# Performance work log

Hardware: AMD Instinct MI355X
Metric: run time of the kernel (lower is better)

Reference implementation:

```python
import jax, jax.numpy as jnp
import numpy as np

DIM = 768
NH = 12
HID = int(DIM * 1.5)  # 1152
B_, T_, W_ = 8, 8, 14
HW = 14 * 14
N = HW + 1
BT = B_ * T_


def _ln(x, g, b, eps=1e-5):
    m = jnp.mean(x, axis=-1, keepdims=True)
    v = jnp.var(x, axis=-1, keepdims=True)
    return (x - m) / jnp.sqrt(v + eps) * g + b


def _attn(x, wqkv, wproj, bproj, nh):
    # manual q@k^T -> softmax -> @v, as in the torch module (no qkv bias)
    b, n, c = x.shape
    hd = c // nh
    scale = hd ** -0.5
    qkv = (x @ wqkv.T).reshape(b, n, 3, nh, hd).transpose(2, 0, 3, 1, 4)
    q, k, v = qkv[0], qkv[1], qkv[2]
    a = jax.nn.softmax(jnp.einsum('bhnd,bhmd->bhnm', q, k) * scale, axis=-1)
    o = jnp.einsum('bhnm,bhmd->bhnd', a, v).transpose(0, 2, 1, 3).reshape(b, n, c)
    return o @ wproj.T + bproj


def setup_inputs() -> dict:
    key = jax.random.key(0)
    ks = jax.random.split(key, 16)
    s = 0.02
    d = {
        'x': jax.random.normal(ks[0], (BT, N, DIM), jnp.float32),
        'ln1_g': jnp.ones((DIM,), jnp.float32),
        'ln1_b': jnp.zeros((DIM,), jnp.float32),
        'qkv_w': jax.random.normal(ks[1], (3 * DIM, DIM), jnp.float32) * s,
        'proj_w': jax.random.normal(ks[2], (DIM, DIM), jnp.float32) * s,
        'proj_b': jnp.zeros((DIM,), jnp.float32),
        'tln_g': jnp.ones((DIM,), jnp.float32),
        'tln_b': jnp.zeros((DIM,), jnp.float32),
        'tqkv_w': jax.random.normal(ks[3], (3 * DIM, DIM), jnp.float32) * s,
        'tproj_w': jax.random.normal(ks[4], (DIM, DIM), jnp.float32) * s,
        'tproj_b': jnp.zeros((DIM,), jnp.float32),
        # module zero-inits temporal_fc; use small random so the branch is exercised
        'tfc_w': jax.random.normal(ks[5], (DIM, DIM), jnp.float32) * s,
        'tfc_b': jnp.zeros((DIM,), jnp.float32),
        'ln2_g': jnp.ones((DIM,), jnp.float32),
        'ln2_b': jnp.zeros((DIM,), jnp.float32),
        'fc1_w': jax.random.normal(ks[6], (HID, DIM), jnp.float32) * s,
        'fc1_b': jnp.zeros((HID,), jnp.float32),
        'fc2_w': jax.random.normal(ks[7], (DIM, HID), jnp.float32) * s,
        'fc2_b': jnp.zeros((DIM,), jnp.float32),
        'B': B_, 'T': T_, 'W': W_,
    }
    return d


def reference(x, ln1_g, ln1_b, qkv_w, proj_w, proj_b,
              tln_g, tln_b, tqkv_w, tproj_w, tproj_b, tfc_w, tfc_b,
              ln2_g, ln2_b, fc1_w, fc1_b, fc2_w, fc2_b, B, T, W):
    bt, n, c = x.shape
    hw = n - 1  # spatial tokens (cls excluded)
    # temporal branch: (b t) hw m -> (b hw) t m
    xt = x[:, 1:, :].reshape(B, T, hw, c).transpose(0, 2, 1, 3).reshape(B * hw, T, c)
    xt = _attn(_ln(xt, tln_g, tln_b), tqkv_w, tproj_w, tproj_b, NH)
    xt = xt.reshape(B, hw, T, c).transpose(0, 2, 1, 3).reshape(bt, hw, c)
    xt = xt @ tfc_w.T + tfc_b
    x = x.at[:, 1:, :].add(xt)  # in-place += in torch
    # spatial attention + residual
    x = x + _attn(_ln(x, ln1_g, ln1_b), qkv_w, proj_w, proj_b, NH)
    # MLP + residual (exact GELU, matching nn.GELU default)
    h = jax.nn.gelu(_ln(x, ln2_g, ln2_b) @ fc1_w.T + fc1_b, approximate=False)
    x = x + (h @ fc2_w.T + fc2_b)
    return x
```

## Files before the change

kernel.cpp:

```cpp
#include <hip/hip_runtime.h>
#include <hip/hip_bf16.h>


#define DIM   768
#define NH    12
#define HD    64
#define HID   1152
#define B_    8
#define T_    8
#define HW_   196
#define NTOK  197
#define BT_   64
#define MROWS (BT_ * NTOK)
#define TROWS (B_ * HW_ * T_)

typedef __bf16 bf16x8 __attribute__((ext_vector_type(8)));
typedef float  f32x4  __attribute__((ext_vector_type(4)));

__device__ inline float bf2f(ushort u) { return __uint_as_float(((unsigned)u) << 16); }
__device__ inline ushort f2bf(float f) {
    unsigned u = __float_as_uint(f);
    unsigned r = (u + 0x7fffu + ((u >> 16) & 1u)) >> 16;
    return (ushort)r;
}

__device__ inline float wred_sum(float v) {
    #pragma unroll
    for (int m = 32; m; m >>= 1) v += __shfl_xor(v, m);
    return v;
}

__device__ __forceinline__ void gload_lds16(const void* g, void* l) {
    __builtin_amdgcn_global_load_lds(
        (const __attribute__((address_space(1))) unsigned int*)g,
        (__attribute__((address_space(3))) unsigned int*)l, 16, 0, 0);
}

__device__ __forceinline__ int xcd_lin(int gid, int nwg) {
    int q = nwg >> 3, r = nwg & 7;
    int xcd = gid & 7, idx = gid >> 3;
    return (xcd < r ? xcd * (q + 1) : r * (q + 1) + (xcd - r) * q) + idx;
}

#define MFMA16(a, b, c) __builtin_amdgcn_mfma_f32_16x16x32_bf16(a, b, c, 0, 0, 0)

__global__ __launch_bounds__(256) void cast_all(
    const float* s0, ushort* d0, int c0, const float* s1, ushort* d1, int c1,
    const float* s2, ushort* d2, int c2, const float* s3, ushort* d3, int c3,
    const float* s4, ushort* d4, int c4, const float* s5, ushort* d5, int c5,
    const float* s6, ushort* d6, int c6)
{
    int i = blockIdx.x * 256 + threadIdx.x;
    const float* s; ushort* d; int base;
    if      (i < c0) { s = s0; d = d0; base = 0;  }
    else if (i < c1) { s = s1; d = d1; base = c0; }
    else if (i < c2) { s = s2; d = d2; base = c1; }
    else if (i < c3) { s = s3; d = d3; base = c2; }
    else if (i < c4) { s = s4; d = d4; base = c3; }
    else if (i < c5) { s = s5; d = d5; base = c4; }
    else if (i < c6) { s = s6; d = d6; base = c5; }
    else return;
    int k = i - base;
    float4 a = *(const float4*)(s + (size_t)k * 8);
    float4 b = *(const float4*)(s + (size_t)k * 8 + 4);
    ushort o[8] = {f2bf(a.x), f2bf(a.y), f2bf(a.z), f2bf(a.w),
                   f2bf(b.x), f2bf(b.y), f2bf(b.z), f2bf(b.w)};
    *(uint4*)(d + (size_t)k * 8) = *(const uint4*)o;
}

__global__ __launch_bounds__(256) void init_cls(const float* __restrict__ x, float* __restrict__ out)
{
    int i = blockIdx.x * 256 + threadIdx.x;
    int r = i / 192, c = (i % 192) * 4;
    size_t off = ((size_t)r * NTOK) * DIM + c;
    *(float4*)(out + off) = *(const float4*)(x + off);
}

template <int KK>
__global__ __launch_bounds__(512, 1) void gemm256(
    const ushort* __restrict__ Ag, const ushort* __restrict__ Wg,
    ushort* __restrict__ Cg, int M, int N, int nm, int nn, int grp)
{
    __shared__ ushort As[2][256 * 64];
    __shared__ ushort Bs[2][256 * 64];

    const int tid  = threadIdx.x;
    const int lane = tid & 63, wid = tid >> 6;
    const int wr = wid >> 2, wc = wid & 3;
    const int fr = lane & 15, fq = lane >> 4;

    int lin = xcd_lin(blockIdx.x, nm * nn);
    int per = grp * nn;
    int g2 = lin / per, rem = lin % per;
    int bm = g2 * grp;
    int gm = nm - bm; if (gm > grp) gm = grp;
    const int m0 = (bm + rem % gm) * 256;
    const int n0 = (rem / gm) * 256;

    const int srow = wid * 8 + (lane >> 3);
    const int scol = 8 * ((lane & 7) ^ (lane >> 3));
    const ushort* aP[4]; const ushort* bP[4];
    #pragma unroll
    for (int j = 0; j < 4; ++j) {
        int ra = m0 + j * 64 + srow; if (ra >= M) ra = M - 1;
        aP[j] = Ag + (size_t)ra * KK + scol;
        bP[j] = Wg + (size_t)(n0 + j * 64 + srow) * KK + scol;
    }
    const int ldso = (wid * 8) * 64;

    f32x4 acc[8][4] = {};
    bf16x8 af[4][2], b0[2][2], b1[2][2];

    const int sw0 = (fq * 8) ^ ((fr & 7) * 8);
    const int sw1 = (32 + fq * 8) ^ ((fr & 7) * 8);

    #pragma unroll
    for (int j = 0; j < 4; ++j) gload_lds16(aP[j], &As[0][j * 4096 + ldso]);
    #pragma unroll
    for (int j = 0; j < 4; ++j) gload_lds16(bP[j], &Bs[0][j * 4096 + ldso]);

    constexpr int NT = KK / 64;
    #pragma unroll
    for (int t = 0; t < NT; ++t) {
        const int rb = t & 1, wb = rb ^ 1;
        const bool st = (t + 1 < NT);
        const int kw = (t + 1) * 64;

        asm volatile("s_waitcnt vmcnt(0)" ::: "memory");
        __builtin_amdgcn_s_barrier();
        __builtin_amdgcn_sched_barrier(0);

        #pragma unroll
        for (int mf = 0; mf < 4; ++mf) {
            af[mf][0] = *(const bf16x8*)&As[rb][(wr * 128 + mf * 16 + fr) * 64 + sw0];
            af[mf][1] = *(const bf16x8*)&As[rb][(wr * 128 + mf * 16 + fr) * 64 + sw1];
        }
        #pragma unroll
        for (int nf = 0; nf < 2; ++nf) {
            b0[nf][0] = *(const bf16x8*)&Bs[rb][(wc * 64 + nf * 16 + fr) * 64 + sw0];
            b0[nf][1] = *(const bf16x8*)&Bs[rb][(wc * 64 + nf * 16 + fr) * 64 + sw1];
        }
        if (st) {
            #pragma unroll
            for (int j = 0; j < 4; ++j) gload_lds16(aP[j] + kw, &As[wb][j * 4096 + ldso]);
        }
        asm volatile("s_waitcnt lgkmcnt(0)" ::: "memory");
        __builtin_amdgcn_sched_barrier(0);
        __builtin_amdgcn_s_setprio(1);
        #pragma unroll
        for (int mf = 0; mf < 4; ++mf)
            #pragma unroll
            for (int nf = 0; nf < 2; ++nf) {
                acc[mf][nf] = MFMA16(af[mf][0], b0[nf][0], acc[mf][nf]);
                acc[mf][nf] = MFMA16(af[mf][1], b0[nf][1], acc[mf][nf]);
            }
        __builtin_amdgcn_s_setprio(0);
        __builtin_amdgcn_sched_barrier(0);

        #pragma unroll
        for (int nf = 0; nf < 2; ++nf) {
            b1[nf][0] = *(const bf16x8*)&Bs[rb][(wc * 64 + (nf + 2) * 16 + fr) * 64 + sw0];
            b1[nf][1] = *(const bf16x8*)&Bs[rb][(wc * 64 + (nf + 2) * 16 + fr) * 64 + sw1];
        }
        if (st) {
            #pragma unroll
            for (int j = 0; j < 4; ++j) gload_lds16(bP[j] + kw, &Bs[wb][j * 4096 + ldso]);
        }
        asm volatile("s_waitcnt lgkmcnt(0)" ::: "memory");
        __builtin_amdgcn_sched_barrier(0);
        __builtin_amdgcn_s_setprio(1);
        #pragma unroll
        for (int mf = 0; mf < 4; ++mf)
            #pragma unroll
            for (int nf = 0; nf < 2; ++nf) {
                acc[mf][nf + 2] = MFMA16(af[mf][0], b1[nf][0], acc[mf][nf + 2]);
                acc[mf][nf + 2] = MFMA16(af[mf][1], b1[nf][1], acc[mf][nf + 2]);
            }
        __builtin_amdgcn_s_setprio(0);
        __builtin_amdgcn_sched_barrier(0);

        #pragma unroll
        for (int mf = 0; mf < 4; ++mf) {
            af[mf][0] = *(const bf16x8*)&As[rb][(wr * 128 + 64 + mf * 16 + fr) * 64 + sw0];
            af[mf][1] = *(const bf16x8*)&As[rb][(wr * 128 + 64 + mf * 16 + fr) * 64 + sw1];
        }
        asm volatile("s_waitcnt lgkmcnt(0)" ::: "memory");
        __builtin_amdgcn_sched_barrier(0);
        __builtin_amdgcn_s_setprio(1);
        #pragma unroll
        for (int mf = 0; mf < 4; ++mf)
            #pragma unroll
            for (int nf = 0; nf < 2; ++nf) {
                acc[mf + 4][nf] = MFMA16(af[mf][0], b0[nf][0], acc[mf + 4][nf]);
                acc[mf + 4][nf] = MFMA16(af[mf][1], b0[nf][1], acc[mf + 4][nf]);
            }
        __builtin_amdgcn_s_setprio(0);
        __builtin_amdgcn_sched_barrier(0);

        __builtin_amdgcn_s_setprio(1);
        #pragma unroll
        for (int mf = 0; mf < 4; ++mf)
            #pragma unroll
            for (int nf = 0; nf < 2; ++nf) {
                acc[mf + 4][nf + 2] = MFMA16(af[mf][0], b1[nf][0], acc[mf + 4][nf + 2]);
                acc[mf + 4][nf + 2] = MFMA16(af[mf][1], b1[nf][1], acc[mf + 4][nf + 2]);
            }
        __builtin_amdgcn_s_setprio(0);
        __builtin_amdgcn_sched_barrier(0);
    }

    #pragma unroll
    for (int mf = 0; mf < 8; ++mf)
        #pragma unroll
        for (int e = 0; e < 4; ++e) {
            int row = m0 + wr * 128 + mf * 16 + fq * 4 + e;
            if (row >= M) continue;
            #pragma unroll
            for (int nf = 0; nf < 4; ++nf)
                Cg[(size_t)row * N + n0 + wc * 64 + nf * 16 + fr] = f2bf(acc[mf][nf][e]);
        }
}

enum { EPI_STORE = 0, EPI_BIAS_STORE = 1, EPI_BIAS_GELU = 2, EPI_BIAS_ADD = 3, EPI_BIAS_INIT_TFC = 4 };

template <int EPI, int KK>
__global__ __launch_bounds__(256) void gemm_bt(
    const ushort* __restrict__ Ag, const ushort* __restrict__ Wg,
    const float* __restrict__ bias, ushort* __restrict__ Cg,
    const float* __restrict__ xsrc, float* __restrict__ xf,
    int M, int N, int nm, int nn, int grp)
{
    __shared__ ushort As[2][128 * 64];
    __shared__ ushort Bs[2][128 * 64];

    const int tid  = threadIdx.x;
    const int lane = tid & 63, wid = tid >> 6;

    int lin = xcd_lin(blockIdx.x, nm * nn);
    int per = grp * nn;
    int g2 = lin / per, rem = lin % per;
    int bm = g2 * grp;
    int gm = nm - bm; if (gm > grp) gm = grp;
    const int m0 = (bm + rem % gm) * 128;
    const int n0 = (rem / gm) * 128;

    const int wm = (wid >> 1) * 64, wn = (wid & 1) * 64;
    const int fr = lane & 15, fq = lane >> 4;

    const int srow   = wid * 8 + (lane >> 3);
    const int scolsw = 8 * ((lane & 7) ^ (lane >> 3));
    const ushort* aSrc[4]; const ushort* bSrc[4];
    #pragma unroll
    for (int j = 0; j < 4; ++j) {
        int ra = m0 + j * 32 + srow; if (ra >= M) ra = M - 1;
        aSrc[j] = Ag + (size_t)ra * KK + scolsw;
        bSrc[j] = Wg + (size_t)(n0 + j * 32 + srow) * KK + scolsw;
    }

    f32x4 acc[4][4] = {};

    auto STAGE = [&](int buf, int k0) {
        #pragma unroll
        for (int j = 0; j < 4; ++j) {
            gload_lds16(aSrc[j] + k0, &As[buf][(j * 32 + wid * 8) * 64]);
            gload_lds16(bSrc[j] + k0, &Bs[buf][(j * 32 + wid * 8) * 64]);
        }
    };

    auto COMPUTE = [&](int buf) {
        #pragma unroll
        for (int ks = 0; ks < 2; ++ks) {
            bf16x8 af[4], bfr[4];
            #pragma unroll
            for (int i = 0; i < 4; ++i)
                af[i] = *(const bf16x8*)&As[buf][(wm + i * 16 + fr) * 64 +
                                                ((ks * 32 + fq * 8) ^ ((fr & 7) * 8))];
            #pragma unroll
            for (int j = 0; j < 4; ++j)
                bfr[j] = *(const bf16x8*)&Bs[buf][(wn + j * 16 + fr) * 64 +
                                                 ((ks * 32 + fq * 8) ^ ((fr & 7) * 8))];
            #pragma unroll
            for (int i = 0; i < 4; ++i)
                #pragma unroll
                for (int j = 0; j < 4; ++j)
                    acc[i][j] = MFMA16(af[i], bfr[j], acc[i][j]);
        }
    };

    constexpr int NT = KK / 64;
    STAGE(0, 0);
    STAGE(1, 64);
    #pragma unroll
    for (int t = 0; t < NT; ++t) {
        if (t + 1 < NT) asm volatile("s_waitcnt vmcnt(8)" ::: "memory");
        else asm volatile("s_waitcnt vmcnt(0)" ::: "memory");
        __builtin_amdgcn_s_barrier();
        __builtin_amdgcn_sched_barrier(0);
        COMPUTE(t & 1);
        __builtin_amdgcn_sched_barrier(0);
        __builtin_amdgcn_s_barrier();
        __builtin_amdgcn_sched_barrier(0);
        if (t + 2 < NT) STAGE(t & 1, (t + 2) * 64);
    }

    #pragma unroll
    for (int i = 0; i < 4; ++i) {
        #pragma unroll
        for (int e = 0; e < 4; ++e) {
            int row = m0 + wm + i * 16 + fq * 4 + e;
            if (row >= M) continue;
            #pragma unroll
            for (int j = 0; j < 4; ++j) {
                int col = n0 + wn + j * 16 + fr;
                float v = acc[i][j][e];
                if constexpr (EPI != EPI_STORE) v += bias[col];
                if constexpr (EPI == EPI_BIAS_GELU) v = 0.5f * v * (1.0f + erff(v * 0.70710678118654752f));
                if constexpr (EPI == EPI_STORE || EPI == EPI_BIAS_STORE || EPI == EPI_BIAS_GELU) {
                    Cg[(size_t)row * N + col] = f2bf(v);
                } else if constexpr (EPI == EPI_BIAS_ADD) {
                    xf[(size_t)row * DIM + col] += v;
                } else {
                    int t2 = row & 7, pp = (row >> 3) % HW_, bb = row / (HW_ * T_);
                    size_t dst = ((size_t)(bb * T_ + t2) * NTOK + 1 + pp) * DIM + col;
                    xf[dst] = xsrc[dst] + v;
                }
            }
        }
    }
}

__global__ __launch_bounds__(256) void ln_f32(
    const float* __restrict__ src, const float* __restrict__ g,
    const float* __restrict__ b, ushort* __restrict__ dst, int rows)
{
    int widx = threadIdx.x >> 6, lane = threadIdx.x & 63;
    int r = blockIdx.x * 4 + widx;
    if (r >= rows) return;
    const float* row = src + (size_t)r * DIM;
    float v[12], sum = 0.f, sq = 0.f;
    #pragma unroll
    for (int c = 0; c < 3; ++c) {
        float4 t = *(const float4*)(row + c * 256 + lane * 4);
        v[c*4+0] = t.x; v[c*4+1] = t.y; v[c*4+2] = t.z; v[c*4+3] = t.w;
        sum += t.x + t.y + t.z + t.w;
        sq  += t.x*t.x + t.y*t.y + t.z*t.z + t.w*t.w;
    }
    sum = wred_sum(sum); sq = wred_sum(sq);
    float mean = sum * (1.f / DIM);
    float var  = sq * (1.f / DIM) - mean * mean;
    float rstd = rsqrtf(var + 1e-5f);
    #pragma unroll
    for (int c = 0; c < 3; ++c) {
        int idx = c * 256 + lane * 4;
        float4 gg = *(const float4*)(g + idx);
        float4 bb = *(const float4*)(b + idx);
        ushort4 o;
        o.x = f2bf((v[c*4+0] - mean) * rstd * gg.x + bb.x);
        o.y = f2bf((v[c*4+1] - mean) * rstd * gg.y + bb.y);
        o.z = f2bf((v[c*4+2] - mean) * rstd * gg.z + bb.z);
        o.w = f2bf((v[c*4+3] - mean) * rstd * gg.w + bb.w);
        *(ushort4*)(dst + (size_t)r * DIM + idx) = o;
    }
}

__global__ __launch_bounds__(256) void ln_gather(
    const float* __restrict__ x, const float* __restrict__ g,
    const float* __restrict__ b, ushort* __restrict__ dst, int rows)
{
    int widx = threadIdx.x >> 6, lane = threadIdx.x & 63;
    int r = blockIdx.x * 4 + widx;
    if (r >= rows) return;
    int t = r & 7, pp = (r >> 3) % HW_, bb = r / (HW_ * T_);
    const float* row = x + ((size_t)(bb * T_ + t) * NTOK + 1 + pp) * DIM;
    float v[12], sum = 0.f, sq = 0.f;
    #pragma unroll
    for (int c = 0; c < 3; ++c) {
        float4 t4 = *(const float4*)(row + c * 256 + lane * 4);
        v[c*4+0] = t4.x; v[c*4+1] = t4.y; v[c*4+2] = t4.z; v[c*4+3] = t4.w;
        sum += t4.x + t4.y + t4.z + t4.w;
        sq  += t4.x*t4.x + t4.y*t4.y + t4.z*t4.z + t4.w*t4.w;
    }
    sum = wred_sum(sum); sq = wred_sum(sq);
    float mean = sum * (1.f / DIM);
    float var  = sq * (1.f / DIM) - mean * mean;
    float rstd = rsqrtf(var + 1e-5f);
    #pragma unroll
    for (int c = 0; c < 3; ++c) {
        int idx = c * 256 + lane * 4;
        float4 gg = *(const float4*)(g + idx);
        float4 bb2 = *(const float4*)(b + idx);
        ushort4 o;
        o.x = f2bf((v[c*4+0] - mean) * rstd * gg.x + bb2.x);
        o.y = f2bf((v[c*4+1] - mean) * rstd * gg.y + bb2.y);
        o.z = f2bf((v[c*4+2] - mean) * rstd * gg.z + bb2.z);
        o.w = f2bf((v[c*4+3] - mean) * rstd * gg.w + bb2.w);
        *(ushort4*)(dst + (size_t)r * DIM + idx) = o;
    }
}

__global__ __launch_bounds__(256) void attn_temporal(
    const ushort* __restrict__ qkv, ushort* __restrict__ O)
{
    int widx = threadIdx.x >> 6, lane = threadIdx.x & 63;
    int w = blockIdx.x * 4 + widx;
    int s = w / NH, h = w % NH;
    int qi = lane >> 3, kj = lane & 7;

    const ushort* qrow = qkv + (size_t)(s * 8 + qi) * (3 * DIM) + h * HD;
    const ushort* krow = qkv + (size_t)(s * 8 + kj) * (3 * DIM) + DIM + h * HD;
    float d = 0.f;
    #pragma unroll
    for (int c = 0; c < 8; ++c) {
        uint4 qa = *(const uint4*)(qrow + c * 8);
        uint4 ka = *(const uint4*)(krow + c * 8);
        const ushort* qs = (const ushort*)&qa;
        const ushort* ks = (const ushort*)&ka;
        #pragma unroll
        for (int e = 0; e < 8; ++e) d += bf2f(qs[e]) * bf2f(ks[e]);
    }
    float sc = d * 0.125f;
    float mx = sc;
    #pragma unroll
    for (int m = 4; m; m >>= 1) mx = fmaxf(mx, __shfl_xor(mx, m));
    float p = expf(sc - mx);
    float sum = p;
    #pragma unroll
    for (int m = 4; m; m >>= 1) sum += __shfl_xor(sum, m);
    p /= sum;

    float o[8] = {};
    int base = lane & ~7;
    #pragma unroll
    for (int t = 0; t < 8; ++t) {
        float pt = __shfl(p, base + t);
        const ushort* vrow = qkv + (size_t)(s * 8 + t) * (3 * DIM) + 2 * DIM + h * HD + kj * 8;
        uint4 va = *(const uint4*)vrow;
        const ushort* vs = (const ushort*)&va;
        #pragma unroll
        for (int e = 0; e < 8; ++e) o[e] += pt * bf2f(vs[e]);
    }
    ushort out[8];
    #pragma unroll
    for (int e = 0; e < 8; ++e) out[e] = f2bf(o[e]);
    *(uint4*)(O + (size_t)(s * 8 + qi) * DIM + h * HD + kj * 8) = *(const uint4*)out;
}

#define KS_STRIDE 72
#define VT_STRIDE 208
#define P_STRIDE  208
#define KS_OFF    0
#define VT_OFF    (197 * KS_STRIDE)
#define P_OFF     (VT_OFF + 64 * VT_STRIDE)
#define LDS_TOT   (P_OFF + 4 * 16 * P_STRIDE)

__global__ __launch_bounds__(256, 2) void attn_spatial_mfma(
    const ushort* __restrict__ qkv, ushort* __restrict__ O)
{
    __shared__ ushort lds[LDS_TOT];
    const int tid = threadIdx.x, lane = tid & 63, wid = tid >> 6;
    const int fr = lane & 15, fq = lane >> 4;
    int lin = xcd_lin(blockIdx.x, BT_ * NH);
    const int s = lin / NH, h = lin % NH;
    const size_t base = (size_t)s * NTOK * (3 * DIM);
    const ushort* Qg = qkv + base + h * HD;
    const ushort* Kg = qkv + base + DIM + h * HD;
    const ushort* Vg = qkv + base + 2 * DIM + h * HD;

    for (int chunk = tid; chunk < NTOK * 8; chunk += 256) {
        int r = chunk >> 3, c = (chunk & 7) * 8;
        uint4 v = *(const uint4*)(Kg + (size_t)r * (3 * DIM) + c);
        *(uint4*)&lds[KS_OFF + r * KS_STRIDE + c] = v;
    }
    for (int chunk = tid; chunk < 208 * 8; chunk += 256) {
        int k = chunk >> 3, c = (chunk & 7) * 8;
        uint4 v = {0u, 0u, 0u, 0u};
        if (k < NTOK) v = *(const uint4*)(Vg + (size_t)k * (3 * DIM) + c);
        const ushort* e = (const ushort*)&v;
        #pragma unroll
        for (int j = 0; j < 8; ++j) lds[VT_OFF + (c + j) * VT_STRIDE + k] = e[j];
    }
    __syncthreads();

    ushort* P = &lds[P_OFF + wid * 16 * P_STRIDE];

    for (int qi = wid; qi < 13; qi += 4) {
        int qrow = qi * 16 + fr; if (qrow > NTOK - 1) qrow = NTOK - 1;
        bf16x8 qf0 = *(const bf16x8*)(Qg + (size_t)qrow * (3 * DIM) + fq * 8);
        bf16x8 qf1 = *(const bf16x8*)(Qg + (size_t)qrow * (3 * DIM) + 32 + fq * 8);

        f32x4 sacc[13];
        #pragma unroll
        for (int t = 0; t < 13; ++t) {
            bf16x8 kf0 = *(const bf16x8*)&lds[KS_OFF + (t * 16 + fr) * KS_STRIDE + fq * 8];
            bf16x8 kf1 = *(const bf16x8*)&lds[KS_OFF + (t * 16 + fr) * KS_STRIDE + 32 + fq * 8];
            f32x4 z = {0.f, 0.f, 0.f, 0.f};
            z = MFMA16(kf0, qf0, z);
            sacc[t] = MFMA16(kf1, qf1, z);
        }

        float m = -1e30f;
        #pragma unroll
        for (int t = 0; t < 13; ++t)
            #pragma unroll
            for (int e = 0; e < 4; ++e) {
                int k = t * 16 + fq * 4 + e;
                float v = (k < NTOK) ? sacc[t][e] * 0.125f : -1e30f;
                sacc[t][e] = v;
                m = fmaxf(m, v);
            }
        m = fmaxf(m, __shfl_xor(m, 16));
        m = fmaxf(m, __shfl_xor(m, 32));
        float sum = 0.f;
        #pragma unroll
        for (int t = 0; t < 13; ++t)
            #pragma unroll
            for (int e = 0; e < 4; ++e) {
                float p = expf(sacc[t][e] - m);
                sacc[t][e] = p;
                sum += p;
            }
        sum += __shfl_xor(sum, 16);
        sum += __shfl_xor(sum, 32);
        float rd = 1.f / sum;

        #pragma unroll
        for (int t = 0; t < 13; ++t) {
            ushort2 w0 = { f2bf(sacc[t][0] * rd), f2bf(sacc[t][1] * rd) };
            ushort2 w1 = { f2bf(sacc[t][2] * rd), f2bf(sacc[t][3] * rd) };
            *(ushort2*)&P[fr * P_STRIDE + t * 16 + fq * 4]     = w0;
            *(ushort2*)&P[fr * P_STRIDE + t * 16 + fq * 4 + 2] = w1;
        }

        f32x4 oacc[4] = {};
        #pragma unroll
        for (int st = 0; st < 6; ++st) {
            bf16x8 pf = *(const bf16x8*)&P[fr * P_STRIDE + st * 32 + fq * 8];
            #pragma unroll
            for (int dt = 0; dt < 4; ++dt) {
                bf16x8 vf = *(const bf16x8*)&lds[VT_OFF + (dt * 16 + fr) * VT_STRIDE + st * 32 + fq * 8];
                oacc[dt] = MFMA16(pf, vf, oacc[dt]);
            }
        }
        {
            bf16x8 zz = {};
            bf16x8 pf = zz;
            if (fq < 2) pf = *(const bf16x8*)&P[fr * P_STRIDE + 192 + fq * 8];
            #pragma unroll
            for (int dt = 0; dt < 4; ++dt) {
                bf16x8 vf = zz;
                if (fq < 2) vf = *(const bf16x8*)&lds[VT_OFF + (dt * 16 + fr) * VT_STRIDE + 192 + fq * 8];
                oacc[dt] = MFMA16(pf, vf, oacc[dt]);
            }
        }

        #pragma unroll
        for (int dt = 0; dt < 4; ++dt)
            #pragma unroll
            for (int e = 0; e < 4; ++e) {
                int q = qi * 16 + fq * 4 + e;
                if (q < NTOK)
                    O[(size_t)(s * NTOK + q) * DIM + h * HD + dt * 16 + fr] = f2bf(oacc[dt][e]);
            }
    }
}

extern "C" void kernel_launch(void* const* d_in, const int* in_sizes, int n_in,
                              void* d_out, int out_size, void* d_ws, size_t ws_size,
                              hipStream_t stream)
{
    const float* x      = (const float*)d_in[0];
    const float* ln1_g  = (const float*)d_in[1];
    const float* ln1_b  = (const float*)d_in[2];
    const float* qkv_w  = (const float*)d_in[3];
    const float* proj_w = (const float*)d_in[4];
    const float* proj_b = (const float*)d_in[5];
    const float* tln_g  = (const float*)d_in[6];
    const float* tln_b  = (const float*)d_in[7];
    const float* tqkv_w = (const float*)d_in[8];
    const float* tproj_w= (const float*)d_in[9];
    const float* tproj_b= (const float*)d_in[10];
    const float* tfc_w  = (const float*)d_in[11];
    const float* tfc_b  = (const float*)d_in[12];
    const float* ln2_g  = (const float*)d_in[13];
    const float* ln2_b  = (const float*)d_in[14];
    const float* fc1_w  = (const float*)d_in[15];
    const float* fc1_b  = (const float*)d_in[16];
    const float* fc2_w  = (const float*)d_in[17];
    const float* fc2_b  = (const float*)d_in[18];

    float* out = (float*)d_out;

    char* p = (char*)d_ws;
    ushort* w_qkv  = (ushort*)p; p += (size_t)(3*DIM*DIM) * 2;
    ushort* w_proj = (ushort*)p; p += (size_t)(DIM*DIM) * 2;
    ushort* w_tqkv = (ushort*)p; p += (size_t)(3*DIM*DIM) * 2;
    ushort* w_tproj= (ushort*)p; p += (size_t)(DIM*DIM) * 2;
    ushort* w_tfc  = (ushort*)p; p += (size_t)(DIM*DIM) * 2;
    ushort* w_fc1  = (ushort*)p; p += (size_t)(HID*DIM) * 2;
    ushort* w_fc2  = (ushort*)p; p += (size_t)(HID*DIM) * 2;
    ushort* bufA   = (ushort*)p; p += (size_t)MROWS * DIM * 2;
    ushort* bufC   = (ushort*)p; p += (size_t)MROWS * DIM * 2;
    ushort* bufB   = (ushort*)p;

    {
        const int DD8 = DIM * DIM / 8;
        int c0 = 3 * DD8;
        int c1 = c0 + DD8;
        int c2 = c1 + 3 * DD8;
        int c3 = c2 + DD8;
        int c4 = c3 + DD8;
        int c5 = c4 + HID * DIM / 8;
        int c6 = c5 + HID * DIM / 8;
        cast_all<<<dim3((c6 + 255) / 256), dim3(256), 0, stream>>>(
            qkv_w, w_qkv, c0, proj_w, w_proj, c1, tqkv_w, w_tqkv, c2,
            tproj_w, w_tproj, c3, tfc_w, w_tfc, c4, fc1_w, w_fc1, c5,
            fc2_w, w_fc2, c6);
    }

    init_cls<<<dim3(48), dim3(256), 0, stream>>>(x, out);

    #define GEMM(EPI, KV, A, W, BIAS, C, XS, XF, M, N, GRP) \
        gemm_bt<EPI, KV><<<dim3((((M) + 127) / 128) * ((N) / 128)), dim3(256), 0, stream>>>( \
            A, W, BIAS, C, XS, XF, M, N, ((M) + 127) / 128, (N) / 128, GRP)
    #define GEMM256(KV, A, W, C, M, N, GRP) \
        gemm256<KV><<<dim3((((M) + 255) / 256) * ((N) / 256)), dim3(512), 0, stream>>>( \
            A, W, C, M, N, ((M) + 255) / 256, (N) / 256, GRP)

    ln_gather<<<dim3(TROWS / 4), dim3(256), 0, stream>>>(x, tln_g, tln_b, bufA, TROWS);
    GEMM256(DIM, bufA, w_tqkv, bufB, TROWS, 3 * DIM, 1);
    attn_temporal<<<dim3(TROWS * NH / 8 / 4), dim3(256), 0, stream>>>(bufB, bufC);
    GEMM(EPI_BIAS_STORE, DIM, bufC, w_tproj, tproj_b, bufA, nullptr, nullptr, TROWS, DIM, 8);
    GEMM(EPI_BIAS_INIT_TFC, DIM, bufA, w_tfc, tfc_b, nullptr, x, out, TROWS, DIM, 8);

    ln_f32<<<dim3((MROWS + 3) / 4), dim3(256), 0, stream>>>(out, ln1_g, ln1_b, bufA, MROWS);
    GEMM256(DIM, bufA, w_qkv, bufB, MROWS, 3 * DIM, 1);
    attn_spatial_mfma<<<dim3(BT_ * NH), dim3(256), 0, stream>>>(bufB, bufC);
    GEMM(EPI_BIAS_ADD, DIM, bufC, w_proj, proj_b, nullptr, nullptr, out, MROWS, DIM, 8);

    ln_f32<<<dim3((MROWS + 3) / 4), dim3(256), 0, stream>>>(out, ln2_g, ln2_b, bufA, MROWS);
    GEMM(EPI_BIAS_GELU, DIM, bufA, w_fc1, fc1_b, bufB, nullptr, nullptr, MROWS, HID, 8);
    GEMM(EPI_BIAS_ADD, HID, bufB, w_fc2, fc2_b, nullptr, nullptr, out, MROWS, DIM, 4);
    #undef GEMM
    #undef GEMM256
}
```

Before: 415.5 us.

## Fold temporal proj into tfc weight and route all GEMMs through 256-tile kernel

Precomputes a combined weight W_tfc·W_tproj and a combined bias so the temporal projection and temporal_fc GEMMs collapse into one GEMM. It also drops the 128-tile gemm_bt kernel and runs every GEMM through the 256x256 kernel with fused epilogues. The MLP hidden size is zero-padded to 1280 so it divides the 256 tile. This removes one full TROWS x 768 x 768 GEMM and its intermediate buffer. The cost is extra per-call weight preprocessing (a transpose, a small GEMM, padding kernels), slightly changed bf16 rounding, and wasted compute on the padded hidden columns.

```diff
diff --git a/kernel.cpp b/kernel.cpp
--- a/kernel.cpp
+++ b/kernel.cpp
@@ -6,6 +6,7 @@
 #define NH    12
 #define HD    64
 #define HID   1152
+#define HIDP  1280
 #define B_    8
 #define T_    8
 #define HW_   196
@@ -47,8 +48,7 @@
 __global__ __launch_bounds__(256) void cast_all(
     const float* s0, ushort* d0, int c0, const float* s1, ushort* d1, int c1,
     const float* s2, ushort* d2, int c2, const float* s3, ushort* d3, int c3,
-    const float* s4, ushort* d4, int c4, const float* s5, ushort* d5, int c5,
-    const float* s6, ushort* d6, int c6)
+    const float* s4, ushort* d4, int c4)
 {
     int i = blockIdx.x * 256 + threadIdx.x;
     const float* s; ushort* d; int base;
@@ -57,8 +57,6 @@
     else if (i < c2) { s = s2; d = d2; base = c1; }
     else if (i < c3) { s = s3; d = d3; base = c2; }
     else if (i < c4) { s = s4; d = d4; base = c3; }
-    else if (i < c5) { s = s5; d = d5; base = c4; }
-    else if (i < c6) { s = s6; d = d6; base = c5; }
     else return;
     int k = i - base;
     float4 a = *(const float4*)(s + (size_t)k * 8);
@@ -68,6 +66,55 @@
     *(uint4*)(d + (size_t)k * 8) = *(const uint4*)o;
 }
 
+__global__ __launch_bounds__(256) void transpose_cast(const float* __restrict__ in, ushort* __restrict__ out)
+{
+    __shared__ float t[32][33];
+    int bx = blockIdx.x % 24, by = blockIdx.x / 24;
+    int lx = threadIdx.x & 31, ly = threadIdx.x >> 5;
+    #pragma unroll
+    for (int i = 0; i < 32; i += 8)
+        t[ly + i][lx] = in[(size_t)(by * 32 + ly + i) * DIM + bx * 32 + lx];
+    __syncthreads();
+    #pragma unroll
+    for (int i = 0; i < 32; i += 8)
+        out[(size_t)(bx * 32 + ly + i) * DIM + by * 32 + lx] = f2bf(t[lx][ly + i]);
+}
+
+__global__ __launch_bounds__(256) void cast_pad_fc2(const float* __restrict__ in, ushort* __restrict__ out)
+{
+    int i = blockIdx.x * 256 + threadIdx.x;
+    if (i >= DIM * (HIDP / 8)) return;
+    int r = i / (HIDP / 8), c8 = (i % (HIDP / 8)) * 8;
+    ushort o[8];
+    if (c8 < HID) {
+        const float* s = in + (size_t)r * HID + c8;
+        #pragma unroll
+        for (int e = 0; e < 8; ++e) o[e] = f2bf(s[e]);
+    } else {
+        #pragma unroll
+        for (int e = 0; e < 8; ++e) o[e] = 0;
+    }
+    *(uint4*)(out + (size_t)r * HIDP + c8) = *(const uint4*)o;
+}
+
+__global__ __launch_bounds__(256) void pad_bias(const float* __restrict__ in, float* __restrict__ out)
+{
+    int i = blockIdx.x * 256 + threadIdx.x;
+    if (i < HIDP) out[i] = (i < HID) ? in[i] : 0.f;
+}
+
+__global__ __launch_bounds__(256) void bias_comb(
+    const float* __restrict__ tfc_w, const float* __restrict__ tproj_b,
+    const float* __restrict__ tfc_b, float* __restrict__ bc)
+{
+    int w = blockIdx.x * 4 + (threadIdx.x >> 6);
+    int lane = threadIdx.x & 63;
+    float s = 0.f;
+    for (int j = lane; j < DIM; j += 64) s += tfc_w[(size_t)w * DIM + j] * tproj_b[j];
+    s = wred_sum(s);
+    if (lane == 0) bc[w] = s + tfc_b[w];
+}
+
 __global__ __launch_bounds__(256) void init_cls(const float* __restrict__ x, float* __restrict__ out)
 {
     int i = blockIdx.x * 256 + threadIdx.x;
@@ -76,10 +123,14 @@
     *(float4*)(out + off) = *(const float4*)(x + off);
 }
 
-template <int KK>
+enum { EPI_STORE = 0, EPI_BIAS_GELU = 1, EPI_BIAS_ADD = 2, EPI_INIT_TFC = 3 };
+
+template <int KK, int EPI>
 __global__ __launch_bounds__(512, 1) void gemm256(
     const ushort* __restrict__ Ag, const ushort* __restrict__ Wg,
-    ushort* __restrict__ Cg, int M, int N, int nm, int nn, int grp)
+    const float* __restrict__ bias, ushort* __restrict__ Cg,
+    const float* __restrict__ xsrc, float* __restrict__ xf,
+    int M, int N, int nm, int nn, int grp)
 {
     __shared__ ushort As[2][256 * 64];
     __shared__ ushort Bs[2][256 * 64];
@@ -215,118 +266,26 @@
         for (int e = 0; e < 4; ++e) {
             int row = m0 + wr * 128 + mf * 16 + fq * 4 + e;
             if (row >= M) continue;
-            #pragma unroll
-            for (int nf = 0; nf < 4; ++nf)
-                Cg[(size_t)row * N + n0 + wc * 64 + nf * 16 + fr] = f2bf(acc[mf][nf][e]);
-        }
-}
-
-enum { EPI_STORE = 0, EPI_BIAS_STORE = 1, EPI_BIAS_GELU = 2, EPI_BIAS_ADD = 3, EPI_BIAS_INIT_TFC = 4 };
-
-template <int EPI, int KK>
-__global__ __launch_bounds__(256) void gemm_bt(
-    const ushort* __restrict__ Ag, const ushort* __restrict__ Wg,
-    const float* __restrict__ bias, ushort* __restrict__ Cg,
-    const float* __restrict__ xsrc, float* __restrict__ xf,
-    int M, int N, int nm, int nn, int grp)
-{
-    __shared__ ushort As[2][128 * 64];
-    __shared__ ushort Bs[2][128 * 64];
-
-    const int tid  = threadIdx.x;
-    const int lane = tid & 63, wid = tid >> 6;
-
-    int lin = xcd_lin(blockIdx.x, nm * nn);
-    int per = grp * nn;
-    int g2 = lin / per, rem = lin % per;
-    int bm = g2 * grp;
-    int gm = nm - bm; if (gm > grp) gm = grp;
-    const int m0 = (bm + rem % gm) * 128;
-    const int n0 = (rem / gm) * 128;
-
-    const int wm = (wid >> 1) * 64, wn = (wid & 1) * 64;
-    const int fr = lane & 15, fq = lane >> 4;
-
-    const int srow   = wid * 8 + (lane >> 3);
-    const int scolsw = 8 * ((lane & 7) ^ (lane >> 3));
-    const ushort* aSrc[4]; const ushort* bSrc[4];
-    #pragma unroll
-    for (int j = 0; j < 4; ++j) {
-        int ra = m0 + j * 32 + srow; if (ra >= M) ra = M - 1;
-        aSrc[j] = Ag + (size_t)ra * KK + scolsw;
-        bSrc[j] = Wg + (size_t)(n0 + j * 32 + srow) * KK + scolsw;
-    }
-
-    f32x4 acc[4][4] = {};
-
-    auto STAGE = [&](int buf, int k0) {
-        #pragma unroll
-        for (int j = 0; j < 4; ++j) {
-            gload_lds16(aSrc[j] + k0, &As[buf][(j * 32 + wid * 8) * 64]);
-            gload_lds16(bSrc[j] + k0, &Bs[buf][(j * 32 + wid * 8) * 64]);
-        }
-    };
-
-    auto COMPUTE = [&](int buf) {
-        #pragma unroll
-        for (int ks = 0; ks < 2; ++ks) {
-            bf16x8 af[4], bfr[4];
-            #pragma unroll
-            for (int i = 0; i < 4; ++i)
-                af[i] = *(const bf16x8*)&As[buf][(wm + i * 16 + fr) * 64 +
-                                                ((ks * 32 + fq * 8) ^ ((fr & 7) * 8))];
-            #pragma unroll
-            for (int j = 0; j < 4; ++j)
-                bfr[j] = *(const bf16x8*)&Bs[buf][(wn + j * 16 + fr) * 64 +
-                                                 ((ks * 32 + fq * 8) ^ ((fr & 7) * 8))];
-            #pragma unroll
-            for (int i = 0; i < 4; ++i)
-                #pragma unroll
-                for (int j = 0; j < 4; ++j)
-                    acc[i][j] = MFMA16(af[i], bfr[j], acc[i][j]);
-        }
-    };
-
-    constexpr int NT = KK / 64;
-    STAGE(0, 0);
-    STAGE(1, 64);
-    #pragma unroll
-    for (int t = 0; t < NT; ++t) {
-        if (t + 1 < NT) asm volatile("s_waitcnt vmcnt(8)" ::: "memory");
-        else asm volatile("s_waitcnt vmcnt(0)" ::: "memory");
-        __builtin_amdgcn_s_barrier();
-        __builtin_amdgcn_sched_barrier(0);
-        COMPUTE(t & 1);
-        __builtin_amdgcn_sched_barrier(0);
-        __builtin_amdgcn_s_barrier();
-        __builtin_amdgcn_sched_barrier(0);
-        if (t + 2 < NT) STAGE(t & 1, (t + 2) * 64);
-    }
-
-    #pragma unroll
-    for (int i = 0; i < 4; ++i) {
-        #pragma unroll
-        for (int e = 0; e < 4; ++e) {
-            int row = m0 + wm + i * 16 + fq * 4 + e;
-            if (row >= M) continue;
-            #pragma unroll
-            for (int j = 0; j < 4; ++j) {
-                int col = n0 + wn + j * 16 + fr;
-                float v = acc[i][j][e];
+            size_t dstrow = 0;
+            if constexpr (EPI == EPI_INIT_TFC) {
+                int t2 = row & 7, pp = (row >> 3) % HW_, bb = row / (HW_ * T_);
+                dstrow = ((size_t)(bb * T_ + t2) * NTOK + 1 + pp) * DIM;
+            }
+            #pragma unroll
+            for (int nf = 0; nf < 4; ++nf) {
+                int col = n0 + wc * 64 + nf * 16 + fr;
+                float v = acc[mf][nf][e];
                 if constexpr (EPI != EPI_STORE) v += bias[col];
                 if constexpr (EPI == EPI_BIAS_GELU) v = 0.5f * v * (1.0f + erff(v * 0.70710678118654752f));
-                if constexpr (EPI == EPI_STORE || EPI == EPI_BIAS_STORE || EPI == EPI_BIAS_GELU) {
+                if constexpr (EPI == EPI_STORE || EPI == EPI_BIAS_GELU) {
                     Cg[(size_t)row * N + col] = f2bf(v);
                 } else if constexpr (EPI == EPI_BIAS_ADD) {
                     xf[(size_t)row * DIM + col] += v;
                 } else {
-                    int t2 = row & 7, pp = (row >> 3) % HW_, bb = row / (HW_ * T_);
-                    size_t dst = ((size_t)(bb * T_ + t2) * NTOK + 1 + pp) * DIM + col;
-                    xf[dst] = xsrc[dst] + v;
+                    xf[dstrow + col] = xsrc[dstrow + col] + v;
                 }
             }
         }
-    }
 }
 
 __global__ __launch_bounds__(256) void ln_f32(
@@ -594,10 +553,13 @@
     ushort* w_qkv  = (ushort*)p; p += (size_t)(3*DIM*DIM) * 2;
     ushort* w_proj = (ushort*)p; p += (size_t)(DIM*DIM) * 2;
     ushort* w_tqkv = (ushort*)p; p += (size_t)(3*DIM*DIM) * 2;
-    ushort* w_tproj= (ushort*)p; p += (size_t)(DIM*DIM) * 2;
     ushort* w_tfc  = (ushort*)p; p += (size_t)(DIM*DIM) * 2;
-    ushort* w_fc1  = (ushort*)p; p += (size_t)(HID*DIM) * 2;
-    ushort* w_fc2  = (ushort*)p; p += (size_t)(HID*DIM) * 2;
+    ushort* tprojT = (ushort*)p; p += (size_t)(DIM*DIM) * 2;
+    ushort* w_comb = (ushort*)p; p += (size_t)(DIM*DIM) * 2;
+    ushort* w_fc1p = (ushort*)p; p += (size_t)(HIDP*DIM) * 2;
+    ushort* w_fc2p = (ushort*)p; p += (size_t)(DIM*HIDP) * 2;
+    float*  b_comb = (float*)p;  p += DIM * 4;
+    float*  fc1_bp = (float*)p;  p += HIDP * 4;
     ushort* bufA   = (ushort*)p; p += (size_t)MROWS * DIM * 2;
     ushort* bufC   = (ushort*)p; p += (size_t)MROWS * DIM * 2;
     ushort* bufB   = (ushort*)p;
@@ -608,38 +570,36 @@
         int c1 = c0 + DD8;
         int c2 = c1 + 3 * DD8;
         int c3 = c2 + DD8;
-        int c4 = c3 + DD8;
-        int c5 = c4 + HID * DIM / 8;
-        int c6 = c5 + HID * DIM / 8;
-        cast_all<<<dim3((c6 + 255) / 256), dim3(256), 0, stream>>>(
+        int c4 = c3 + HID * DIM / 8;
+        cast_all<<<dim3((c4 + 255) / 256), dim3(256), 0, stream>>>(
             qkv_w, w_qkv, c0, proj_w, w_proj, c1, tqkv_w, w_tqkv, c2,
-            tproj_w, w_tproj, c3, tfc_w, w_tfc, c4, fc1_w, w_fc1, c5,
-            fc2_w, w_fc2, c6);
-    }
-
+            tfc_w, w_tfc, c3, fc1_w, w_fc1p, c4);
+    }
+    hipMemsetAsync(w_fc1p + (size_t)HID * DIM, 0, (size_t)(HIDP - HID) * DIM * 2, stream);
+    transpose_cast<<<dim3(576), dim3(256), 0, stream>>>(tproj_w, tprojT);
+    cast_pad_fc2<<<dim3((DIM * (HIDP / 8) + 255) / 256), dim3(256), 0, stream>>>(fc2_w, w_fc2p);
+    pad_bias<<<dim3((HIDP + 255) / 256), dim3(256), 0, stream>>>(fc1_b, fc1_bp);
+    bias_comb<<<dim3(DIM / 4), dim3(256), 0, stream>>>(tfc_w, tproj_b, tfc_b, b_comb);
     init_cls<<<dim3(48), dim3(256), 0, stream>>>(x, out);
 
-    #define GEMM(EPI, KV, A, W, BIAS, C, XS, XF, M, N, GRP) \
-        gemm_bt<EPI, KV><<<dim3((((M) + 127) / 128) * ((N) / 128)), dim3(256), 0, stream>>>( \
-            A, W, BIAS, C, XS, XF, M, N, ((M) + 127) / 128, (N) / 128, GRP)
-    #define GEMM256(KV, A, W, C, M, N, GRP) \
-        gemm256<KV><<<dim3((((M) + 255) / 256) * ((N) / 256)), dim3(512), 0, stream>>>( \
-            A, W, C, M, N, ((M) + 255) / 256, (N) / 256, GRP)
+    #define GEMM256(KV, EPI, A, W, BIAS, C, XS, XF, M, N, GRP) \
+        gemm256<KV, EPI><<<dim3((((M) + 255) / 256) * ((N) / 256)), dim3(512), 0, stream>>>( \
+            A, W, BIAS, C, XS, XF, M, N, ((M) + 255) / 256, (N) / 256, GRP)
+
+    GEMM256(DIM, EPI_STORE, w_tfc, tprojT, nullptr, w_comb, nullptr, nullptr, DIM, DIM, 1);
 
     ln_gather<<<dim3(TROWS / 4), dim3(256), 0, stream>>>(x, tln_g, tln_b, bufA, TROWS);
-    GEMM256(DIM, bufA, w_tqkv, bufB, TROWS, 3 * DIM, 1);
+    GEMM256(DIM, EPI_STORE, bufA, w_tqkv, nullptr, bufB, nullptr, nullptr, TROWS, 3 * DIM, 1);
     attn_temporal<<<dim3(TROWS * NH / 8 / 4), dim3(256), 0, stream>>>(bufB, bufC);
-    GEMM(EPI_BIAS_STORE, DIM, bufC, w_tproj, tproj_b, bufA, nullptr, nullptr, TROWS, DIM, 8);
-    GEMM(EPI_BIAS_INIT_TFC, DIM, bufA, w_tfc, tfc_b, nullptr, x, out, TROWS, DIM, 8);
+    GEMM256(DIM, EPI_INIT_TFC, bufC, w_comb, b_comb, nullptr, x, out, TROWS, DIM, 1);
 
     ln_f32<<<dim3((MROWS + 3) / 4), dim3(256), 0, stream>>>(out, ln1_g, ln1_b, bufA, MROWS);
-    GEMM256(DIM, bufA, w_qkv, bufB, MROWS, 3 * DIM, 1);
+    GEMM256(DIM, EPI_STORE, bufA, w_qkv, nullptr, bufB, nullptr, nullptr, MROWS, 3 * DIM, 1);
     attn_spatial_mfma<<<dim3(BT_ * NH), dim3(256), 0, stream>>>(bufB, bufC);
-    GEMM(EPI_BIAS_ADD, DIM, bufC, w_proj, proj_b, nullptr, nullptr, out, MROWS, DIM, 8);
+    GEMM256(DIM, EPI_BIAS_ADD, bufC, w_proj, proj_b, nullptr, nullptr, out, MROWS, DIM, 1);
 
     ln_f32<<<dim3((MROWS + 3) / 4), dim3(256), 0, stream>>>(out, ln2_g, ln2_b, bufA, MROWS);
-    GEMM(EPI_BIAS_GELU, DIM, bufA, w_fc1, fc1_b, bufB, nullptr, nullptr, MROWS, HID, 8);
-    GEMM(EPI_BIAS_ADD, HID, bufB, w_fc2, fc2_b, nullptr, nullptr, out, MROWS, DIM, 4);
-    #undef GEMM
+    GEMM256(DIM, EPI_BIAS_GELU, bufA, w_fc1p, fc1_bp, bufB, nullptr, nullptr, MROWS, HIDP, 1);
+    GEMM256(HIDP, EPI_BIAS_ADD, bufB, w_fc2p, fc2_b, nullptr, nullptr, out, MROWS, DIM, 1);
     #undef GEMM256
 }
```

After: 412.3 us. Within noise of the previous version (-0.8%).
